# Kernel tuning notes

Hardware: AMD Instinct MI355X
Metric: run time of the kernel (lower is better)

## Reference

```python
import jax, jax.numpy as jnp
import numpy as np
import math

EMBED_DIM = 1024
NUM_HEADS = 16
HEAD_DIM = EMBED_DIM // NUM_HEADS
BLOCK_SIZE = 64
NUM_RAND_BLOCKS = 3
B, L = 2, 2048


def _build_sparse_mask(seq_len, block_size, num_rand_blocks, seed=0):
    """BigBird block-sparse mask: global (first/last block) + window (prev/self/next) + random blocks."""
    nb = seq_len // block_size
    bm = np.zeros((nb, nb), dtype=bool)
    # global: first and last blocks attend to all / are attended by all
    bm[0, :] = True
    bm[:, 0] = True
    bm[-1, :] = True
    bm[:, -1] = True
    # sliding window for interior blocks
    for b in range(1, nb - 1):
        bm[b, max(b - 1, 0):b + 2] = True
    # random blocks for interior blocks (deterministic for reproducibility)
    rng = np.random.default_rng(seed)
    for b in range(1, nb - 1):
        avail = [x for x in range(nb) if x != b]
        picks = rng.permutation(len(avail))[:num_rand_blocks]
        for p in picks:
            bm[b, avail[p]] = True
    # expand block mask to token-level [L, L]
    return np.kron(bm, np.ones((block_size, block_size), dtype=bool))


def setup_inputs() -> dict:
    key = jax.random.key(0)
    k0, k1, k2, k3, k4 = jax.random.split(key, 5)
    hidden_states = jax.random.normal(k0, (B, L, EMBED_DIM), dtype=jnp.float32)
    s = 0.02
    # torch nn.Linear weights have shape [out_features, in_features]
    Wq = jax.random.normal(k1, (EMBED_DIM, EMBED_DIM), dtype=jnp.float32) * s
    Wk = jax.random.normal(k2, (EMBED_DIM, EMBED_DIM), dtype=jnp.float32) * s
    Wv = jax.random.normal(k3, (EMBED_DIM, EMBED_DIM), dtype=jnp.float32) * s
    Wo = jax.random.normal(k4, (EMBED_DIM, EMBED_DIM), dtype=jnp.float32) * s
    sparse_mask = jnp.asarray(_build_sparse_mask(L, BLOCK_SIZE, NUM_RAND_BLOCKS))
    return {"hidden_states": hidden_states, "Wq": Wq, "Wk": Wk, "Wv": Wv,
            "Wo": Wo, "sparse_mask": sparse_mask}


def reference(hidden_states, Wq, Wk, Wv, Wo, sparse_mask):
    Bsz, Lq, D = hidden_states.shape
    H, hd = NUM_HEADS, HEAD_DIM
    # projections (Linear no bias): x @ W.T
    q = (hidden_states @ Wq.T).reshape(Bsz, Lq, H, hd).transpose(0, 2, 1, 3)
    k = (hidden_states @ Wk.T).reshape(Bsz, Lq, H, hd).transpose(0, 2, 1, 3)
    v = (hidden_states @ Wv.T).reshape(Bsz, Lq, H, hd).transpose(0, 2, 1, 3)
    # dense scores with block-sparse mask (matches reference module's math)
    scores = jnp.einsum('bhqd,bhkd->bhqk', q, k) / math.sqrt(hd)  # [B,H,L,L]
    scores = jnp.where(sparse_mask[None, None, :, :], scores, -jnp.inf)
    attn = jax.nn.softmax(scores.astype(jnp.float32), axis=-1).astype(scores.dtype)
    out = jnp.einsum('bhqk,bhkd->bhqd', attn, v)
    out = out.transpose(0, 2, 1, 3).reshape(Bsz, Lq, D)
    out = out @ Wo.T
    return out
```

## Files before the change

kernel.cpp:

```cpp
#include <hip/hip_runtime.h>
#include <hip/hip_bf16.h>
#include <stdint.h>

#define LSEQ   2048
#define DMODEL 1024
#define NHEADS 16
#define HDIM   64
#define NB     32
#define BATCH  2
#define NGRP   38
#define NWG_ATTN (32 * NGRP)

typedef unsigned short u16;
typedef __attribute__((ext_vector_type(8))) __bf16 bf16x8;
typedef __attribute__((ext_vector_type(4))) float f32x4;
typedef __attribute__((ext_vector_type(4))) unsigned int u32x4;
typedef __attribute__((ext_vector_type(4))) u16 u16x4;


__device__ __forceinline__ u16 f2b(float f) {
  unsigned b = __float_as_uint(f);
  return (u16)((b + 0x7FFFu + ((b >> 16) & 1u)) >> 16);
}

__device__ __forceinline__ void lds_dma16(const u16* g, u16* l) {
  __builtin_amdgcn_global_load_lds(
      (__attribute__((address_space(1))) const void*)g,
      (__attribute__((address_space(3))) void*)l, 16, 0, 0);
}

__device__ __forceinline__ bool probe_is_bf16(const void* src) {
  const u16* p = (const u16*)src;
  int cnt = 0;
  #pragma unroll
  for (int i = 0; i < 64; ++i) {
    int e = (p[i] >> 7) & 0xFF;
    cnt += (e >= 100 && e <= 140) ? 1 : 0;
  }
  return cnt >= 48;
}

__device__ __forceinline__ bool mask_block(const void* m, int qb, int kb) {
  const unsigned char* p = (const unsigned char*)m;
  size_t e = (size_t)(qb * 64) * LSEQ + (size_t)kb * 64;
  unsigned char b0 = p[0], b1 = p[1], b2 = p[2];
  if (b0 == 1 && b1 == 1) return p[e] != 0;
  if (b0 == 1 && b1 == 0 && b2 == 1) return ((const u16*)m)[e] != 0;
  if (b0 == 1) return ((const unsigned int*)m)[e] != 0;
  if (b0 == 0x80 && b1 == 0x3f) return ((const u16*)m)[e] != 0;
  return ((const float*)m)[e] != 0.0f;
}

__global__ __launch_bounds__(256) void convert_kernel(
    const void* __restrict__ hs, const void* __restrict__ wq,
    const void* __restrict__ wk, const void* __restrict__ wv,
    const void* __restrict__ wo, u16* __restrict__ dst,
    const void* __restrict__ mask, int* __restrict__ skb,
    f32x4* __restrict__ zbuf, int zn4) {
  __shared__ int sflag;
  if (threadIdx.x == 0) sflag = probe_is_bf16(hs) ? 1 : 0;
  __syncthreads();
  bool isbf = sflag != 0;
  if (blockIdx.x == 0 && threadIdx.x < NB) {
    int qb = threadIdx.x;
    int base = (qb == 0) ? 0 : ((qb == 31) ? 32 : (64 + (qb - 1) * 8));
    int cap = (qb == 0 || qb == 31) ? 32 : 8;
    int c = 0;
    for (int kb = 0; kb < NB; ++kb)
      if (mask_block(mask, qb, kb)) skb[base + c++] = kb;
    for (; c < cap; ++c) skb[base + c] = -1;
  }
  const int HS4 = BATCH * LSEQ * DMODEL / 4;
  const int W4 = DMODEL * DMODEL / 4;
  int total4 = HS4 + 4 * W4;
  int stride = gridDim.x * blockDim.x;
  for (int i = blockIdx.x * blockDim.x + threadIdx.x; i < total4; i += stride) {
    const void* src;
    int off;
    if (i < HS4) { src = hs; off = i; }
    else {
      int j = i - HS4;
      int wsel = j >> 18;
      off = j & (W4 - 1);
      src = (wsel == 0) ? wq : (wsel == 1) ? wk : (wsel == 2) ? wv : wo;
    }
    u16x4 v;
    if (isbf) v = ((const u16x4*)src)[off];
    else {
      f32x4 f = ((const f32x4*)src)[off];
      v = (u16x4){f2b(f[0]), f2b(f[1]), f2b(f[2]), f2b(f[3])};
    }
    ((u16x4*)dst)[i] = v;
  }
  for (int i = blockIdx.x * blockDim.x + threadIdx.x; i < zn4; i += stride)
    zbuf[i] = (f32x4){0.f, 0.f, 0.f, 0.f};
}

#define GTM 128
#define GTN 128
#define GBK 32
#define LDSW 32

__global__ __launch_bounds__(256) void gemm_bt(
    const u16* __restrict__ A, const u16* __restrict__ Bw,
    void* __restrict__ C, u16* __restrict__ C2, int M, int N, int K,
    int layout, int is_final, const void* __restrict__ probe_src) {
  __shared__ u16 lA[GTM * LDSW];
  __shared__ u16 lB[GTN * LDSW];
  __shared__ int sflag;
  int t = threadIdx.x;
  int w = t >> 6, l = t & 63, q4 = l >> 4, lc = l & 15;
  int lr = l >> 2, lcc = l & 3;
  int tileM = blockIdx.x * GTM, tileN = blockIdx.y * GTN;
  int wm = (w >> 1) * 64, wn = (w & 1) * 64;
  if (t == 0) sflag = (is_final && !probe_is_bf16(probe_src)) ? 0 : 1;

  f32x4 acc[4][4] = {};

  for (int kt = 0; kt < K; kt += GBK) {
    __syncthreads();
    #pragma unroll
    for (int it = 0; it < 2; ++it) {
      int m = w * 2 + it;
      int row = m * 16 + lr;
      lds_dma16(A + (size_t)(tileM + row) * K + kt + lcc * 8, lA + m * 512);
      lds_dma16(Bw + (size_t)(tileN + row) * K + kt + lcc * 8, lB + m * 512);
    }
    __syncthreads();
    bf16x8 af[4], bf[4];
    #pragma unroll
    for (int i = 0; i < 4; ++i)
      af[i] = *(const bf16x8*)(lA + (wm + i * 16 + lc) * LDSW + q4 * 8);
    #pragma unroll
    for (int j = 0; j < 4; ++j)
      bf[j] = *(const bf16x8*)(lB + (wn + j * 16 + lc) * LDSW + q4 * 8);
    #pragma unroll
    for (int i = 0; i < 4; ++i)
      #pragma unroll
      for (int j = 0; j < 4; ++j)
        acc[i][j] = __builtin_amdgcn_mfma_f32_16x16x32_bf16(af[i], bf[j], acc[i][j], 0, 0, 0);
  }

  bool out_bf = sflag != 0;
  #pragma unroll
  for (int i = 0; i < 4; ++i)
    #pragma unroll
    for (int j = 0; j < 4; ++j) {
      int rowb = tileM + wm + i * 16 + q4 * 4;
      int col = tileN + wn + j * 16 + lc;
      if (layout == 0) {
        #pragma unroll
        for (int r = 0; r < 4; ++r) {
          float v = acc[i][j][r];
          size_t idx = (size_t)(rowb + r) * N + col;
          if (out_bf) ((u16*)C)[idx] = f2b(v);
          else ((float*)C)[idx] = v;
        }
      } else {
        int sel = col >> 10;
        int o = col & 1023;
        int h = o >> 6, d = o & 63;
        int b = rowb >> 11, ll = rowb & 2047;
        if (sel == 2) {
          u16x4 pk = {f2b(acc[i][j][0]), f2b(acc[i][j][1]),
                      f2b(acc[i][j][2]), f2b(acc[i][j][3])};
          *(u16x4*)(C2 + ((size_t)((b * NHEADS + h) * HDIM + d)) * LSEQ + ll) = pk;
        } else {
          float sc = (sel == 0) ? 0.125f : 1.0f;
          #pragma unroll
          for (int r = 0; r < 4; ++r) {
            size_t idx = (size_t)sel * (size_t)(BATCH * NHEADS * LSEQ * HDIM) +
                         (((size_t)(b * NHEADS + h) * LSEQ) + ll + r) * HDIM + d;
            ((u16*)C)[idx] = f2b(acc[i][j][r] * sc);
          }
        }
      }
    }
}

#define LDP 72

__global__ __launch_bounds__(256) void attn_kernel(
    const u16* __restrict__ qb_, const u16* __restrict__ kb_,
    const u16* __restrict__ vt_, const int* __restrict__ skb,
    float* __restrict__ obuf2, float* __restrict__ lbuf2,
    u16* __restrict__ ctx) {
  __shared__ u16 lK[64 * 64];
  __shared__ u16 lV[64 * 64];
  __shared__ u16 lP[4][16 * LDP];
  int i = blockIdx.x;
  int bh = (i & 7) + ((i >> 3) & 3) * 8;
  int g = i >> 5;
  int qb = (g < 4) ? 0 : ((g < 8) ? 31 : (g - 7));
  int t = threadIdx.x, w = t >> 6, l = t & 63, q4 = l >> 4, lc = l & 15;
  int c0 = t, c1 = 256 + t;
  int r0 = c0 >> 3, cc0 = c0 & 7, r1 = c1 >> 3, cc1 = c1 & 7;

  const u16* qp = qb_ + ((size_t)bh * LSEQ + qb * 64 + w * 16 + lc) * HDIM;
  bf16x8 bq0 = *(const bf16x8*)(qp + q4 * 8);
  bf16x8 bq1 = *(const bf16x8*)(qp + 32 + q4 * 8);

  const u16* kp = kb_ + (size_t)bh * LSEQ * HDIM;
  const u16* vp = vt_ + (size_t)bh * HDIM * LSEQ;
  u16* myP = &lP[w][0];

  f32x4 oacc[4];
  #pragma unroll
  for (int d = 0; d < 4; ++d) oacc[d] = (f32x4){0.f, 0.f, 0.f, 0.f};
  float lp = 0.0f;

  for (int it = 0; it < 8; ++it) {
    int kb = skb[g * 8 + it];
    if (kb < 0) break;
    const u16* kblk = kp + (size_t)kb * 64 * HDIM;
    const u16* vblk = vp + kb * 64;
    __syncthreads();
    lds_dma16(kblk + r0 * HDIM + cc0 * 8, lK + w * 512);
    lds_dma16(kblk + r1 * HDIM + cc1 * 8, lK + 2048 + w * 512);
    lds_dma16(vblk + (size_t)r0 * LSEQ + cc0 * 8, lV + w * 512);
    lds_dma16(vblk + (size_t)r1 * LSEQ + cc1 * 8, lV + 2048 + w * 512);
    __syncthreads();

    f32x4 st[4];
    #pragma unroll
    for (int mt = 0; mt < 4; ++mt) {
      bf16x8 k0 = *(const bf16x8*)(lK + (mt * 16 + lc) * 64 + q4 * 8);
      bf16x8 k1 = *(const bf16x8*)(lK + (mt * 16 + lc) * 64 + 32 + q4 * 8);
      f32x4 z = (f32x4){0.f, 0.f, 0.f, 0.f};
      z = __builtin_amdgcn_mfma_f32_16x16x32_bf16(k0, bq0, z, 0, 0, 0);
      z = __builtin_amdgcn_mfma_f32_16x16x32_bf16(k1, bq1, z, 0, 0, 0);
      st[mt] = z;
    }

    #pragma unroll
    for (int mt = 0; mt < 4; ++mt) {
      float p0 = __expf(st[mt][0]), p1 = __expf(st[mt][1]);
      float p2 = __expf(st[mt][2]), p3 = __expf(st[mt][3]);
      lp += (p0 + p1) + (p2 + p3);
      u16x4 pk = {f2b(p0), f2b(p1), f2b(p2), f2b(p3)};
      *(u16x4*)(myP + lc * LDP + mt * 16 + q4 * 4) = pk;
    }

    bf16x8 ap0 = *(const bf16x8*)(myP + lc * LDP + q4 * 8);
    bf16x8 ap1 = *(const bf16x8*)(myP + lc * LDP + 32 + q4 * 8);
    #pragma unroll
    for (int dt = 0; dt < 4; ++dt) {
      bf16x8 v0 = *(const bf16x8*)(lV + (dt * 16 + lc) * 64 + q4 * 8);
      bf16x8 v1 = *(const bf16x8*)(lV + (dt * 16 + lc) * 64 + 32 + q4 * 8);
      oacc[dt] = __builtin_amdgcn_mfma_f32_16x16x32_bf16(ap0, v0, oacc[dt], 0, 0, 0);
      oacc[dt] = __builtin_amdgcn_mfma_f32_16x16x32_bf16(ap1, v1, oacc[dt], 0, 0, 0);
    }
  }

  float ltot = lp;
  ltot += __shfl_xor(ltot, 16);
  ltot += __shfl_xor(ltot, 32);

  if (g >= 8) {
    float inv[4];
    #pragma unroll
    for (int r = 0; r < 4; ++r)
      inv[r] = 1.0f / __shfl(ltot, q4 * 4 + r);
    int b = bh >> 4, h = bh & 15;
    #pragma unroll
    for (int dt = 0; dt < 4; ++dt)
      #pragma unroll
      for (int r = 0; r < 4; ++r) {
        float v = oacc[dt][r] * inv[r];
        int grow = qb * 64 + w * 16 + q4 * 4 + r;
        size_t odx = ((size_t)b * LSEQ + grow) * DMODEL + h * HDIM + dt * 16 + lc;
        ctx[odx] = f2b(v);
      }
  } else {
    int s = (qb == 31) ? 1 : 0;
    if (q4 == 0)
      unsafeAtomicAdd(lbuf2 + ((size_t)bh * 2 + s) * 64 + w * 16 + lc, ltot);
    #pragma unroll
    for (int dt = 0; dt < 4; ++dt)
      #pragma unroll
      for (int r = 0; r < 4; ++r)
        unsafeAtomicAdd(obuf2 + (((size_t)bh * 2 + s) * 64 + w * 16 + q4 * 4 + r) * 64 +
                            dt * 16 + lc, oacc[dt][r]);
  }
}

__global__ __launch_bounds__(256) void normalize2_kernel(
    const float* __restrict__ obuf2, const float* __restrict__ lbuf2,
    u16* __restrict__ ctx) {
  int e4 = blockIdx.x * 256 + threadIdx.x;
  int e = e4 * 4;
  int bh = e >> 13;
  int rem = e & 8191;
  int s = rem >> 12, row = (rem >> 6) & 63, d = rem & 63;
  f32x4 o = *(const f32x4*)(obuf2 + e);
  float linv = 1.0f / lbuf2[(bh * 2 + s) * 64 + row];
  int qb = s ? 31 : 0;
  int b = bh >> 4, h = bh & 15;
  int grow = qb * 64 + row;
  u16x4 pk = {f2b(o[0] * linv), f2b(o[1] * linv), f2b(o[2] * linv), f2b(o[3] * linv)};
  *(u16x4*)(ctx + ((size_t)b * LSEQ + grow) * DMODEL + h * HDIM + d) = pk;
}

extern "C" void kernel_launch(void* const* d_in, const int* in_sizes, int n_in,
                              void* d_out, int out_size, void* d_ws, size_t ws_size,
                              hipStream_t stream) {
  const void* hs = d_in[0];
  const void* wq = d_in[1];
  const void* wk = d_in[2];
  const void* wv = d_in[3];
  const void* wo = d_in[4];
  const void* mask = d_in[5];

  u16* hsb = (u16*)d_ws;
  u16* wqb = hsb + 4 * 1024 * 1024;
  u16* wob = wqb + 3 * 1024 * 1024;
  u16* qbuf = wob + 1024 * 1024;
  u16* kbuf = qbuf + 4 * 1024 * 1024;
  u16* vtb  = kbuf + 4 * 1024 * 1024;
  u16* ctx  = vtb + 4 * 1024 * 1024;
  int* skb  = (int*)(ctx + 4 * 1024 * 1024);
  float* obuf2 = (float*)(skb + 512);
  float* lbuf2 = obuf2 + 32 * 2 * 64 * 64;
  const int ZN4 = (32 * 2 * 64 * 64 + 4096) / 4;

  convert_kernel<<<4096, 256, 0, stream>>>(hs, wq, wk, wv, wo, hsb, mask, skb,
                                           (f32x4*)obuf2, ZN4);

  dim3 gqkv(32, 24);
  gemm_bt<<<gqkv, 256, 0, stream>>>(hsb, wqb, qbuf, vtb, 4096, 3072, 1024, 1, 0, hs);

  attn_kernel<<<NWG_ATTN, 256, 0, stream>>>(qbuf, kbuf, vtb, skb, obuf2, lbuf2, ctx);

  normalize2_kernel<<<256, 256, 0, stream>>>(obuf2, lbuf2, ctx);

  dim3 gout(32, 8);
  gemm_bt<<<gout, 256, 0, stream>>>(ctx, wob, d_out, nullptr, 4096, 1024, 1024, 0, 1, hs);
}
```

Baseline: 216.6 us.

## Add dedicated 256x256 QKV GEMM with LDS-DMA double-buffered pipeline

Replaces the generic 128x128 gemm_bt for the QKV projection with a specialized 256x256x64 tile kernel using 512 threads, direct global-to-LDS DMA loads, double-buffered staging interleaved with MFMA phases, and setprio around MFMA bursts. Larger tiles raise arithmetic intensity and the staged schedule aims to overlap memory loads with compute. It needs 128KB dynamic LDS and launches only 192 workgroups, which may underfill the GPU's compute units and relies on hardcoded K=1024 shapes.

```diff
diff --git a/kernel.cpp b/kernel.cpp
--- a/kernel.cpp
+++ b/kernel.cpp
@@ -94,6 +94,145 @@
   }
   for (int i = blockIdx.x * blockDim.x + threadIdx.x; i < zn4; i += stride)
     zbuf[i] = (f32x4){0.f, 0.f, 0.f, 0.f};
+}
+
+#define QBM 256
+#define QBN 256
+#define QBK 64
+
+#define BAR()  __builtin_amdgcn_s_barrier()
+#define LGK0() asm volatile("s_waitcnt lgkmcnt(0)" ::: "memory")
+#define VM4()  asm volatile("s_waitcnt vmcnt(4)" ::: "memory")
+#define VM0()  asm volatile("s_waitcnt vmcnt(0)" ::: "memory")
+
+#define STG_A(p, h, kt) do { \
+    lds_dma16(Abase + ((h)*128 +  0)*1024 + (kt)*64, sA + (p)*16384 + (h)*8192 +        wb8); \
+    lds_dma16(Abase + ((h)*128 + 64)*1024 + (kt)*64, sA + (p)*16384 + (h)*8192 + 4096 + wb8); \
+  } while (0)
+#define STG_B(p, h, kt) do { \
+    lds_dma16(Bbase + ((h)*128 +  0)*1024 + (kt)*64, sB + (p)*16384 + (h)*8192 +        wb8); \
+    lds_dma16(Bbase + ((h)*128 + 64)*1024 + (kt)*64, sB + (p)*16384 + (h)*8192 + 4096 + wb8); \
+  } while (0)
+
+#define LDA(p, mh) do { \
+    const u16* _ba = sA + (p)*16384 + (wr*128 + (mh)*64 + lc)*64 + q4*8; \
+    af[0][0] = *(const bf16x8*)(_ba       ); af[0][1] = *(const bf16x8*)(_ba +   32); \
+    af[1][0] = *(const bf16x8*)(_ba + 1024); af[1][1] = *(const bf16x8*)(_ba + 1056); \
+    af[2][0] = *(const bf16x8*)(_ba + 2048); af[2][1] = *(const bf16x8*)(_ba + 2080); \
+    af[3][0] = *(const bf16x8*)(_ba + 3072); af[3][1] = *(const bf16x8*)(_ba + 3104); \
+  } while (0)
+#define LDB(p, nh) do { \
+    const u16* _bb = sB + (p)*16384 + (wc*64 + (nh)*32 + lc)*64 + q4*8; \
+    bfr[nh][0][0] = *(const bf16x8*)(_bb       ); bfr[nh][0][1] = *(const bf16x8*)(_bb +   32); \
+    bfr[nh][1][0] = *(const bf16x8*)(_bb + 1024); bfr[nh][1][1] = *(const bf16x8*)(_bb + 1056); \
+  } while (0)
+
+#define MMQ(mh, nh) do { \
+    __builtin_amdgcn_s_setprio(1); \
+    _Pragma("unroll") \
+    for (int _m = 0; _m < 4; ++_m) { \
+      _Pragma("unroll") \
+      for (int _n = 0; _n < 2; ++_n) { \
+        f32x4 _c = acc[(mh)*4+_m][(nh)*2+_n]; \
+        _c = __builtin_amdgcn_mfma_f32_16x16x32_bf16(af[_m][0], bfr[nh][_n][0], _c, 0, 0, 0); \
+        _c = __builtin_amdgcn_mfma_f32_16x16x32_bf16(af[_m][1], bfr[nh][_n][1], _c, 0, 0, 0); \
+        acc[(mh)*4+_m][(nh)*2+_n] = _c; \
+      } \
+    } \
+    __builtin_amdgcn_s_setprio(0); \
+  } while (0)
+
+__global__ __launch_bounds__(512, 2) void gemm_qkv(
+    const u16* __restrict__ A, const u16* __restrict__ Bw,
+    u16* __restrict__ C, u16* __restrict__ C2) {
+  extern __shared__ u16 smem[];
+  u16* sA = smem;
+  u16* sB = smem + 2 * 16384;
+
+  const int t = threadIdx.x;
+  const int l = t & 63;
+  const int w = t >> 6;
+  const int wr = w >> 2;
+  const int wc = w & 3;
+  const int q4 = l >> 4, lc = l & 15;
+  const int tileM = blockIdx.x * QBM;
+  const int tileN = blockIdx.y * QBN;
+  const int sr = t >> 3;
+  const int sc = (t & 7) * 8;
+  const int wb8 = w * 512;
+
+  const u16* Abase = A + (size_t)(tileM + sr) * 1024 + sc;
+  const u16* Bbase = Bw + (size_t)(tileN + sr) * 1024 + sc;
+
+  f32x4 acc[8][4] = {};
+  bf16x8 af[4][2];
+  bf16x8 bfr[2][2][2];
+
+  STG_B(0, 0, 0); STG_B(0, 1, 0);
+  STG_A(0, 0, 0); STG_A(0, 1, 0);
+  STG_B(1, 0, 1); STG_B(1, 1, 1);
+  VM4(); BAR();
+
+  #pragma unroll 1
+  for (int j = 0; j < 7; ++j) {
+    const int kt0 = 2 * j, kt1 = 2 * j + 1;
+    LDA(0, 0); LDB(0, 0); STG_A(1, 0, kt1);
+    BAR(); LGK0(); MMQ(0, 0); BAR();
+    LDB(0, 1); STG_A(1, 1, kt1);
+    BAR(); LGK0(); MMQ(0, 1); BAR();
+    LDA(0, 1); STG_B(0, 0, kt0 + 2);
+    BAR(); LGK0(); MMQ(1, 1); BAR();
+    STG_B(0, 1, kt0 + 2);
+    VM4(); BAR(); MMQ(1, 0); BAR();
+    LDA(1, 0); LDB(1, 0); STG_A(0, 0, kt0 + 2);
+    BAR(); LGK0(); MMQ(0, 0); BAR();
+    LDB(1, 1); STG_A(0, 1, kt0 + 2);
+    BAR(); LGK0(); MMQ(0, 1); BAR();
+    LDA(1, 1); STG_B(1, 0, kt1 + 2);
+    BAR(); LGK0(); MMQ(1, 1); BAR();
+    STG_B(1, 1, kt1 + 2);
+    VM4(); BAR(); MMQ(1, 0); BAR();
+  }
+
+  LDA(0, 0); LDB(0, 0); STG_A(1, 0, 15);
+  BAR(); LGK0(); MMQ(0, 0); BAR();
+  LDB(0, 1); STG_A(1, 1, 15);
+  BAR(); LGK0(); MMQ(0, 1); BAR();
+  LDA(0, 1);
+  BAR(); LGK0(); MMQ(1, 1); BAR();
+  VM0(); BAR(); MMQ(1, 0); BAR();
+  LDA(1, 0); LDB(1, 0);
+  BAR(); LGK0(); MMQ(0, 0); BAR();
+  LDB(1, 1);
+  BAR(); LGK0(); MMQ(0, 1); BAR();
+  LDA(1, 1);
+  LGK0(); MMQ(1, 1);
+  MMQ(1, 0);
+
+  #pragma unroll
+  for (int im = 0; im < 8; ++im)
+    #pragma unroll
+    for (int jn = 0; jn < 4; ++jn) {
+      int rowb = tileM + wr * 128 + im * 16 + q4 * 4;
+      int col = tileN + wc * 64 + jn * 16 + lc;
+      int sel = col >> 10;
+      int o = col & 1023;
+      int h = o >> 6, d = o & 63;
+      int b = rowb >> 11, ll = rowb & 2047;
+      if (sel == 2) {
+        u16x4 pk = {f2b(acc[im][jn][0]), f2b(acc[im][jn][1]),
+                    f2b(acc[im][jn][2]), f2b(acc[im][jn][3])};
+        *(u16x4*)(C2 + ((size_t)((b * NHEADS + h) * HDIM + d)) * LSEQ + ll) = pk;
+      } else {
+        float scl = (sel == 0) ? 0.125f : 1.0f;
+        #pragma unroll
+        for (int r = 0; r < 4; ++r) {
+          size_t idx = (size_t)sel * (size_t)(BATCH * NHEADS * LSEQ * HDIM) +
+                       (((size_t)(b * NHEADS + h) * LSEQ) + ll + r) * HDIM + d;
+          C[idx] = f2b(acc[im][jn][r] * scl);
+        }
+      }
+    }
 }
 
 #define GTM 128
@@ -323,11 +462,18 @@
   float* lbuf2 = obuf2 + 32 * 2 * 64 * 64;
   const int ZN4 = (32 * 2 * 64 * 64 + 4096) / 4;
 
+  static bool attr_done = false;
+  if (!attr_done) {
+    hipFuncSetAttribute((const void*)gemm_qkv,
+                        hipFuncAttributeMaxDynamicSharedMemorySize, 131072);
+    attr_done = true;
+  }
+
   convert_kernel<<<4096, 256, 0, stream>>>(hs, wq, wk, wv, wo, hsb, mask, skb,
                                            (f32x4*)obuf2, ZN4);
 
-  dim3 gqkv(32, 24);
-  gemm_bt<<<gqkv, 256, 0, stream>>>(hsb, wqb, qbuf, vtb, 4096, 3072, 1024, 1, 0, hs);
+  dim3 gqkv(16, 12);
+  gemm_qkv<<<gqkv, 512, 131072, stream>>>(hsb, wqb, qbuf, vtb);
 
   attn_kernel<<<NWG_ATTN, 256, 0, stream>>>(qbuf, kbuf, vtb, skb, obuf2, lbuf2, ctx);
 
```

Result: no change. 215.6 us (-0.5%).
